# Optimization experiments

Measured on AMD Instinct MI355X. Metric: run time of the kernel, lower is better.

Reference implementation:

```python
import jax, jax.numpy as jnp
import numpy as np

B, T, C, H, HS = 128, 256, 384, 6, 64

def setup_inputs() -> dict:
    key = jax.random.key(0)
    k1, k2, k3, k4, k5 = jax.random.split(key, 5)
    s = 0.02
    return {
        "x": jax.random.normal(k1, (B, T, C), dtype=jnp.float32),
        "Wq": jax.random.normal(k2, (H, C, HS), dtype=jnp.float32) * s,
        "Wk": jax.random.normal(k3, (H, C, HS), dtype=jnp.float32) * s,
        "Wv": jax.random.normal(k4, (H, C, HS), dtype=jnp.float32) * s,
        "Wp": jax.random.normal(k5, (C, C), dtype=jnp.float32) * s,
        "bp": jnp.zeros((C,), dtype=jnp.float32),
    }

def reference(x, Wq, Wk, Wv, Wp, bp):
    # per-head projections: [B,H,T,HS]
    q = jnp.einsum('btc,hcd->bhtd', x, Wq)
    k = jnp.einsum('btc,hcd->bhtd', x, Wk)
    v = jnp.einsum('btc,hcd->bhtd', x, Wv)
    scale = 1.0 / jnp.sqrt(jnp.asarray(HS, dtype=x.dtype))
    # scores: [B,H,T,T], causal mask then stable softmax
    scores = jnp.einsum('bhtd,bhsd->bhts', q, k) * scale
    causal = jnp.tril(jnp.ones((T, T), dtype=bool))
    scores = jnp.where(causal, scores, -jnp.inf)
    wei = jax.nn.softmax(scores, axis=-1)
    # dropout is identity in eval mode
    out = jnp.einsum('bhts,bhsd->bhtd', wei, v)  # [B,H,T,HS]
    out = out.transpose(0, 2, 1, 3).reshape(B, T, H * HS)  # concat heads
    return out @ Wp.T + bp  # output projection
```

## Files before the change

kernel.cpp:

```cpp
#include <hip/hip_runtime.h>
#include <hip/hip_bf16.h>
#include <math.h>

#define B_   128
#define T_   256
#define C_   384
#define H_   6
#define HS_  64
#define NTOK (B_*T_)
#define NQKV (3*C_)

typedef unsigned short u16;
typedef __attribute__((ext_vector_type(8))) short bf16x8;
typedef __attribute__((ext_vector_type(4))) float f32x4;

__device__ __forceinline__ u16 f2b(float f) {
    unsigned int u = __builtin_bit_cast(unsigned int, f);
    unsigned int r = (u + 0x7FFFu + ((u >> 16) & 1u)) >> 16;
    return (u16)r;
}

__device__ __forceinline__ float fexp2(float x) {
#if __has_builtin(__builtin_amdgcn_exp2f)
    return __builtin_amdgcn_exp2f(x);
#else
    return exp2f(x);
#endif
}

__device__ __forceinline__ void gl2lds16(const u16* g, u16* l) {
    __builtin_amdgcn_global_load_lds(
        (const __attribute__((address_space(1))) unsigned int*)g,
        (__attribute__((address_space(3))) unsigned int*)l, 16, 0, 0);
}

#define QSCALE 0.180336880f

#define J0_ (NTOK*C_/8)
#define J2_ (C_*C_/8)
#define J1_ (NQKV*C_)

__global__ __launch_bounds__(256) void prep(
    const float* __restrict__ x,  const float* __restrict__ Wq,
    const float* __restrict__ Wk, const float* __restrict__ Wv,
    const float* __restrict__ Wp,
    u16* __restrict__ xb, u16* __restrict__ wct, u16* __restrict__ wpb)
{
    int i = blockIdx.x * 256 + threadIdx.x;
    if (i < J0_) {
        const float4* s = (const float4*)x + (size_t)i * 2;
        float4 a = s[0], b = s[1];
        ushort4 o1, o2;
        o1.x = f2b(a.x); o1.y = f2b(a.y); o1.z = f2b(a.z); o1.w = f2b(a.w);
        o2.x = f2b(b.x); o2.y = f2b(b.y); o2.z = f2b(b.z); o2.w = f2b(b.w);
        ((ushort4*)xb)[(size_t)i * 2]     = o1;
        ((ushort4*)xb)[(size_t)i * 2 + 1] = o2;
    } else if (i < J0_ + J2_) {
        int j = i - J0_;
        const float4* s = (const float4*)Wp + (size_t)j * 2;
        float4 a = s[0], b = s[1];
        ushort4 o1, o2;
        o1.x = f2b(a.x); o1.y = f2b(a.y); o1.z = f2b(a.z); o1.w = f2b(a.w);
        o2.x = f2b(b.x); o2.y = f2b(b.y); o2.z = f2b(b.z); o2.w = f2b(b.w);
        ((ushort4*)wpb)[(size_t)j * 2]     = o1;
        ((ushort4*)wpb)[(size_t)j * 2 + 1] = o2;
    } else {
        int j = i - J0_ - J2_;
        if (j < J1_) {
            int n = j / C_, c = j % C_;
            int p = n / C_, rem = n % C_;
            int h = rem >> 6, d = rem & 63;
            const float* W = (p == 0 ? Wq : (p == 1 ? Wk : Wv));
            wct[j] = f2b(W[(h * C_ + c) * HS_ + d]);
        }
    }
}

__global__ __launch_bounds__(512, 4) void gemm_qkv(
    const u16* __restrict__ xb, const u16* __restrict__ wct,
    u16* __restrict__ qo, u16* __restrict__ ko, u16* __restrict__ vt)
{
    __shared__ __align__(16) u16 As[256 * 64];
    __shared__ __align__(16) u16 Bs[128 * 64];

    const int gid  = blockIdx.x;
    const int xcd  = gid & 7;
    const int j_   = gid >> 3;
    const int colb = j_ % 9;
    const int rowb = (j_ / 9) * 8 + xcd;
    const int m0g  = rowb * 256;
    const int n0g  = colb * 128;

    const int tid = threadIdx.x;
    const int w = tid >> 6, lane = tid & 63;
    const int lm = lane & 15, qd = lane >> 4;
    const int wm = (w >> 1) * 64, wn = (w & 1) * 64;

    const int schunk = (lane & 7) ^ ((lane >> 3) & 7);
    const u16* gA = xb  + (size_t)(m0g + w * 32 + (lane >> 3)) * C_ + schunk * 8;
    const u16* gB = wct + (size_t)(n0g + w * 16 + (lane >> 3)) * C_ + schunk * 8;
    u16* lA = &As[(w * 32) * 64];
    u16* lB = &Bs[(w * 16) * 64];

    f32x4 acc[4][4];
    #pragma unroll
    for (int mi = 0; mi < 4; ++mi)
        #pragma unroll
        for (int ni = 0; ni < 4; ++ni)
            acc[mi][ni] = (f32x4){0.f, 0.f, 0.f, 0.f};

    for (int k0 = 0; k0 < C_; k0 += 64) {
        __syncthreads();
        #pragma unroll
        for (int j = 0; j < 4; ++j)
            gl2lds16(gA + j * 8 * C_, lA + j * 8 * 64);
        #pragma unroll
        for (int j = 0; j < 2; ++j)
            gl2lds16(gB + j * 8 * C_, lB + j * 8 * 64);
        gA += 64; gB += 64;
        __syncthreads();

        #pragma unroll
        for (int ks = 0; ks < 2; ++ks) {
            bf16x8 af[4], bfr[4];
            #pragma unroll
            for (int mi = 0; mi < 4; ++mi) {
                const int row = wm + mi * 16 + lm;
                const int sl = (ks * 4 + qd) ^ (lm & 7);
                af[mi] = *(const bf16x8*)&As[row * 64 + sl * 8];
            }
            #pragma unroll
            for (int ni = 0; ni < 4; ++ni) {
                const int row = wn + ni * 16 + lm;
                const int sl = (ks * 4 + qd) ^ (lm & 7);
                bfr[ni] = *(const bf16x8*)&Bs[row * 64 + sl * 8];
            }
            #pragma unroll
            for (int mi = 0; mi < 4; ++mi)
                #pragma unroll
                for (int ni = 0; ni < 4; ++ni)
                    acc[mi][ni] = __builtin_amdgcn_mfma_f32_16x16x32_bf16(
                        af[mi], bfr[ni], acc[mi][ni], 0, 0, 0);
        }
    }

    const int bI = m0g >> 8;

    if (colb < 6) {
        u16* dst = (colb < 3) ? qo : ko;
        const float scl = (colb < 3) ? QSCALE : 1.0f;
        const int hBase = (colb % 3) * 2;
        u16 (*tb)[136] = (u16(*)[136])As;
        const int rloc = tid >> 3;
        #pragma unroll
        for (int mi = 0; mi < 4; ++mi) {
            __syncthreads();
            #pragma unroll
            for (int ni = 0; ni < 4; ++ni)
                #pragma unroll
                for (int r = 0; r < 4; ++r)
                    tb[(w >> 1) * 16 + qd * 4 + r][wn + ni * 16 + lm]
                        = f2b(acc[mi][ni][r] * scl);
            __syncthreads();
            const int t = (rloc >> 4) * 64 + mi * 16 + (rloc & 15);
            #pragma unroll
            for (int jj = 0; jj < 2; ++jj) {
                const int cc = (tid & 7) * 8 + jj * 64;
                const int h = hBase + (cc >> 6);
                bf16x8 vv = *(const bf16x8*)&tb[rloc][cc];
                *(bf16x8*)(dst + ((size_t)(bI * H_ + h) * T_ + t) * HS_ + (cc & 63)) = vv;
            }
        }
    } else {
        #pragma unroll
        for (int mi = 0; mi < 4; ++mi) {
            #pragma unroll
            for (int ni = 0; ni < 4; ++ni) {
                const int nn = (colb - 6) * 128 + wn + ni * 16 + lm;
                const int h = nn >> 6, d = nn & 63;
                const int t0 = wm + mi * 16 + qd * 4;
                ushort4 sv;
                sv.x = f2b(acc[mi][ni][0]); sv.y = f2b(acc[mi][ni][1]);
                sv.z = f2b(acc[mi][ni][2]); sv.w = f2b(acc[mi][ni][3]);
                *(ushort4*)(vt + ((size_t)(bI * H_ + h) * HS_ + d) * T_ + t0) = sv;
            }
        }
    }
}

__global__ __launch_bounds__(256, 3) void attn_mfma(
    const u16* __restrict__ q, const u16* __restrict__ k,
    const u16* __restrict__ vt, u16* __restrict__ yb)
{
    __shared__ __align__(16) u16 SM[128 * 64 + 64 * 128 + 4 * 16 * 72];
    u16* Ks = SM;
    u16* Vs = SM + 8192;
    u16* Ps = SM + 16384;

    const int bh = blockIdx.x;
    const int qt = blockIdx.y;
    const int b = bh / H_, h = bh % H_;
    const int tid = threadIdx.x, w = tid >> 6, lane = tid & 63;
    const int lm = lane & 15, qd = lane >> 4;

    const u16* qb = q  + (size_t)bh * T_ * HS_;
    const u16* kb = k  + (size_t)bh * T_ * HS_;
    const u16* vb = vt + (size_t)bh * HS_ * T_;

    const int t0 = qt * 128 + w * 16;

    bf16x8 aq[2][2];
    #pragma unroll
    for (int rg = 0; rg < 2; ++rg) {
        const u16* qrow = qb + (size_t)(t0 + rg * 64 + lm) * HS_;
        aq[rg][0] = *(const bf16x8*)(qrow + qd * 8);
        aq[rg][1] = *(const bf16x8*)(qrow + 32 + qd * 8);
    }

    f32x4 acc[2][4];
    float ms[2][4], ls[2][4];
    #pragma unroll
    for (int rg = 0; rg < 2; ++rg) {
        #pragma unroll
        for (int ni = 0; ni < 4; ++ni) acc[rg][ni] = (f32x4){0.f, 0.f, 0.f, 0.f};
        #pragma unroll
        for (int r = 0; r < 4; ++r) { ms[rg][r] = -INFINITY; ls[rg][r] = 0.f; }
    }

    u16* Pw = &Ps[w * 16 * 72];
    const int nph = qt + 1;

    for (int p = 0; p < nph; ++p) {
        if (p) __syncthreads();
        #pragma unroll
        for (int j = 0; j < 4; ++j) {
            const int row = w * 32 + j * 8 + (lane >> 3);
            const int c = (lane & 7) ^ (row & 7);
            gl2lds16(kb + (size_t)(p * 128 + row) * HS_ + c * 8,
                     &Ks[(w * 32 + j * 8) * 64]);
        }
        #pragma unroll
        for (int j = 0; j < 4; ++j) {
            const int d = w * 16 + j * 4 + (lane >> 4);
            const int c = (lane & 15) ^ (d & 15);
            gl2lds16(vb + (size_t)d * T_ + p * 128 + c * 8,
                     &Vs[(w * 16 + j * 4) * 128]);
        }
        __syncthreads();

        for (int kt2 = 0; kt2 < 2; ++kt2) {
            const int j0 = p * 128 + kt2 * 64;
            #pragma unroll
            for (int rg = 0; rg < 2; ++rg) {
                const int trg = t0 + rg * 64;
                if (j0 > trg + 15) continue;
                const bool needmask = (j0 + 63 > trg);

                f32x4 st[4];
                #pragma unroll
                for (int ni = 0; ni < 4; ++ni) st[ni] = (f32x4){0.f, 0.f, 0.f, 0.f};
                #pragma unroll
                for (int ks = 0; ks < 2; ++ks) {
                    #pragma unroll
                    for (int ni = 0; ni < 4; ++ni) {
                        const int lrow = kt2 * 64 + ni * 16 + lm;
                        const int sl = (ks * 4 + qd) ^ (lm & 7);
                        bf16x8 bk = *(const bf16x8*)&Ks[lrow * 64 + sl * 8];
                        st[ni] = __builtin_amdgcn_mfma_f32_16x16x32_bf16(
                            aq[rg][ks], bk, st[ni], 0, 0, 0);
                    }
                }

                float vals[4][4], rowmax[4];
                #pragma unroll
                for (int r = 0; r < 4; ++r) rowmax[r] = -INFINITY;
                #pragma unroll
                for (int ni = 0; ni < 4; ++ni) {
                    const int s_g = j0 + ni * 16 + lm;
                    #pragma unroll
                    for (int r = 0; r < 4; ++r) {
                        float sc = st[ni][r];
                        if (needmask) {
                            const int t_g = trg + qd * 4 + r;
                            sc = (s_g > t_g) ? -1e30f : sc;
                        }
                        vals[ni][r] = sc;
                        rowmax[r] = fmaxf(rowmax[r], sc);
                    }
                }
                #pragma unroll
                for (int msk = 1; msk <= 8; msk <<= 1)
                    #pragma unroll
                    for (int r = 0; r < 4; ++r)
                        rowmax[r] = fmaxf(rowmax[r], __shfl_xor(rowmax[r], msk, 64));

                float corr[4], rowsum[4];
                #pragma unroll
                for (int r = 0; r < 4; ++r) {
                    const float mn = fmaxf(ms[rg][r], rowmax[r]);
                    corr[r] = fexp2(ms[rg][r] - mn);
                    ms[rg][r] = mn;
                    rowsum[r] = 0.f;
                }
                #pragma unroll
                for (int ni = 0; ni < 4; ++ni) {
                    #pragma unroll
                    for (int r = 0; r < 4; ++r) {
                        const float pv = fexp2(vals[ni][r] - ms[rg][r]);
                        rowsum[r] += pv;
                        Pw[(qd * 4 + r) * 72 + ni * 16 + lm] = f2b(pv);
                    }
                }
                #pragma unroll
                for (int msk = 1; msk <= 8; msk <<= 1)
                    #pragma unroll
                    for (int r = 0; r < 4; ++r)
                        rowsum[r] += __shfl_xor(rowsum[r], msk, 64);
                #pragma unroll
                for (int r = 0; r < 4; ++r) ls[rg][r] = ls[rg][r] * corr[r] + rowsum[r];
                #pragma unroll
                for (int ni = 0; ni < 4; ++ni)
                    #pragma unroll
                    for (int r = 0; r < 4; ++r)
                        acc[rg][ni][r] *= corr[r];

                #pragma unroll
                for (int ks = 0; ks < 2; ++ks) {
                    bf16x8 pa = *(const bf16x8*)&Pw[lm * 72 + ks * 32 + qd * 8];
                    #pragma unroll
                    for (int ni = 0; ni < 4; ++ni) {
                        const int d = ni * 16 + lm;
                        const int c = (kt2 * 8 + ks * 4 + qd) ^ lm;
                        bf16x8 bv = *(const bf16x8*)&Vs[d * 128 + c * 8];
                        acc[rg][ni] = __builtin_amdgcn_mfma_f32_16x16x32_bf16(
                            pa, bv, acc[rg][ni], 0, 0, 0);
                    }
                }
            }
        }
    }

    __syncthreads();
    u16 (*yt)[72] = (u16(*)[72])SM;
    #pragma unroll
    for (int rg = 0; rg < 2; ++rg)
        #pragma unroll
        for (int r = 0; r < 4; ++r) {
            const float inv = 1.f / ls[rg][r];
            #pragma unroll
            for (int ni = 0; ni < 4; ++ni)
                yt[w * 16 + rg * 64 + qd * 4 + r][ni * 16 + lm]
                    = f2b(acc[rg][ni][r] * inv);
        }
    __syncthreads();
    #pragma unroll
    for (int rr = 0; rr < 4; ++rr) {
        const int row = rr * 32 + (tid >> 3);
        const int col = (tid & 7) * 8;
        bf16x8 vv = *(const bf16x8*)&yt[row][col];
        const int t_g = qt * 128 + row;
        *(bf16x8*)(yb + ((size_t)(b * T_ + t_g)) * C_ + h * 64 + col) = vv;
    }
}

__global__ __launch_bounds__(512, 4) void gemm_proj(
    const u16* __restrict__ yb, const u16* __restrict__ wpb,
    const float* __restrict__ bp, float* __restrict__ out)
{
    __shared__ __align__(16) u16 SMEM[256 * 64 + 128 * 64];
    u16* As = SMEM;
    u16* Bs = SMEM + 256 * 64;

    const int gid  = blockIdx.x;
    const int xcd  = gid & 7;
    const int j_   = gid >> 3;
    const int colb = j_ % 3;
    const int rowb = (j_ / 3) * 8 + xcd;
    const int m0g  = rowb * 256;
    const int n0g  = colb * 128;

    const int tid = threadIdx.x;
    const int w = tid >> 6, lane = tid & 63;
    const int lm = lane & 15, qd = lane >> 4;
    const int wm = (w >> 1) * 64, wn = (w & 1) * 64;

    const int schunk = (lane & 7) ^ ((lane >> 3) & 7);
    const u16* gA = yb  + (size_t)(m0g + w * 32 + (lane >> 3)) * C_ + schunk * 8;
    const u16* gB = wpb + (size_t)(n0g + w * 16 + (lane >> 3)) * C_ + schunk * 8;
    u16* lA = &As[(w * 32) * 64];
    u16* lB = &Bs[(w * 16) * 64];

    f32x4 acc[4][4];
    #pragma unroll
    for (int mi = 0; mi < 4; ++mi)
        #pragma unroll
        for (int ni = 0; ni < 4; ++ni)
            acc[mi][ni] = (f32x4){0.f, 0.f, 0.f, 0.f};

    for (int k0 = 0; k0 < C_; k0 += 64) {
        __syncthreads();
        #pragma unroll
        for (int j = 0; j < 4; ++j)
            gl2lds16(gA + j * 8 * C_, lA + j * 8 * 64);
        #pragma unroll
        for (int j = 0; j < 2; ++j)
            gl2lds16(gB + j * 8 * C_, lB + j * 8 * 64);
        gA += 64; gB += 64;
        __syncthreads();

        #pragma unroll
        for (int ks = 0; ks < 2; ++ks) {
            bf16x8 af[4], bfr[4];
            #pragma unroll
            for (int mi = 0; mi < 4; ++mi) {
                const int row = wm + mi * 16 + lm;
                const int sl = (ks * 4 + qd) ^ (lm & 7);
                af[mi] = *(const bf16x8*)&As[row * 64 + sl * 8];
            }
            #pragma unroll
            for (int ni = 0; ni < 4; ++ni) {
                const int row = wn + ni * 16 + lm;
                const int sl = (ks * 4 + qd) ^ (lm & 7);
                bfr[ni] = *(const bf16x8*)&Bs[row * 64 + sl * 8];
            }
            #pragma unroll
            for (int mi = 0; mi < 4; ++mi)
                #pragma unroll
                for (int ni = 0; ni < 4; ++ni)
                    acc[mi][ni] = __builtin_amdgcn_mfma_f32_16x16x32_bf16(
                        af[mi], bfr[ni], acc[mi][ni], 0, 0, 0);
        }
    }

    float bpv[4];
    #pragma unroll
    for (int ni = 0; ni < 4; ++ni) bpv[ni] = bp[n0g + wn + ni * 16 + lm];

    float (*tb)[132] = (float(*)[132])SMEM;
    const int rloc = tid >> 3;
    #pragma unroll
    for (int mi = 0; mi < 4; ++mi) {
        __syncthreads();
        #pragma unroll
        for (int ni = 0; ni < 4; ++ni)
            #pragma unroll
            for (int r = 0; r < 4; ++r)
                tb[(w >> 1) * 16 + qd * 4 + r][wn + ni * 16 + lm]
                    = acc[mi][ni][r] + bpv[ni];
        __syncthreads();
        const int m = m0g + (rloc >> 4) * 64 + mi * 16 + (rloc & 15);
        #pragma unroll
        for (int jj = 0; jj < 4; ++jj) {
            const int cc = (tid & 7) * 4 + jj * 32;
            float4 vv = *(const float4*)&tb[rloc][cc];
            *(float4*)(out + (size_t)m * C_ + n0g + cc) = vv;
        }
    }
}

extern "C" void kernel_launch(void* const* d_in, const int* in_sizes, int n_in,
                              void* d_out, int out_size, void* d_ws, size_t ws_size,
                              hipStream_t stream)
{
    const float* x  = (const float*)d_in[0];
    const float* Wq = (const float*)d_in[1];
    const float* Wk = (const float*)d_in[2];
    const float* Wv = (const float*)d_in[3];
    const float* Wp = (const float*)d_in[4];
    const float* bp = (const float*)d_in[5];
    float* out = (float*)d_out;

    u16* xb  = (u16*)d_ws;
    u16* wct = xb  + (size_t)NTOK * C_;
    u16* wpb = wct + (size_t)NQKV * C_;
    u16* qo  = wpb + (size_t)C_ * C_;
    u16* ko  = qo  + (size_t)B_ * H_ * T_ * HS_;
    u16* vt  = ko  + (size_t)B_ * H_ * T_ * HS_;
    u16* yb  = vt  + (size_t)B_ * H_ * T_ * HS_;

    const int prep_blocks = (J0_ + J2_ + J1_ + 255) / 256;
    hipLaunchKernelGGL(prep, dim3(prep_blocks), dim3(256), 0, stream,
                       x, Wq, Wk, Wv, Wp, xb, wct, wpb);

    hipLaunchKernelGGL(gemm_qkv, dim3((NTOK / 256) * (NQKV / 128)), dim3(512), 0, stream,
                       xb, wct, qo, ko, vt);

    hipLaunchKernelGGL(attn_mfma, dim3(B_ * H_, T_ / 128), dim3(256), 0, stream,
                       qo, ko, vt, yb);

    hipLaunchKernelGGL(gemm_proj, dim3((NTOK / 256) * (C_ / 128)), dim3(512), 0, stream,
                       yb, wpb, bp, out);
}
```

Measured before the change: 197.5 us.

## Fuse QKV projection and causal attention into one per-(batch,head) kernel

Merges the QKV GEMM and the attention kernel so each block computes Q, K and V for one (batch, head) over all 256 tokens. The results stay in shared memory with swizzled layouts instead of round-tripping through global memory. The weight layout is reordered per head (q,k,v contiguous per head) so one block's B tile covers 192 columns. This removes the intermediate Q/K/V global writes and reads and one launch, but uses 96KB of LDS, fewer blocks (768), lower occupancy, and causal imbalance between warps.

```diff
diff --git a/kernel.cpp b/kernel.cpp
--- a/kernel.cpp
+++ b/kernel.cpp
@@ -68,45 +68,43 @@
         int j = i - J0_ - J2_;
         if (j < J1_) {
             int n = j / C_, c = j % C_;
-            int p = n / C_, rem = n % C_;
-            int h = rem >> 6, d = rem & 63;
+            int h = n / 192, rem = n % 192;
+            int p = rem >> 6, d = rem & 63;
             const float* W = (p == 0 ? Wq : (p == 1 ? Wk : Wv));
             wct[j] = f2b(W[(h * C_ + c) * HS_ + d]);
         }
     }
 }
 
-__global__ __launch_bounds__(512, 4) void gemm_qkv(
+__global__ __launch_bounds__(512, 2) void qkv_attn(
     const u16* __restrict__ xb, const u16* __restrict__ wct,
-    u16* __restrict__ qo, u16* __restrict__ ko, u16* __restrict__ vt)
+    u16* __restrict__ yb)
 {
-    __shared__ __align__(16) u16 As[256 * 64];
-    __shared__ __align__(16) u16 Bs[128 * 64];
-
-    const int gid  = blockIdx.x;
-    const int xcd  = gid & 7;
-    const int j_   = gid >> 3;
-    const int colb = j_ % 9;
-    const int rowb = (j_ / 9) * 8 + xcd;
-    const int m0g  = rowb * 256;
-    const int n0g  = colb * 128;
+    __shared__ __align__(16) u16 SM[49152];
+    u16* Qs = SM;
+    u16* Ks = SM + 16384;
+    u16* Vs = SM + 32768;
+
+    const int gid = blockIdx.x;
+    const int lin = (gid & 7) * 96 + (gid >> 3);
+    const int b = lin / 6, h = lin % 6;
 
     const int tid = threadIdx.x;
     const int w = tid >> 6, lane = tid & 63;
     const int lm = lane & 15, qd = lane >> 4;
-    const int wm = (w >> 1) * 64, wn = (w & 1) * 64;
+    const int wm = (w >> 1) * 64, wn = (w & 1) * 96;
 
     const int schunk = (lane & 7) ^ ((lane >> 3) & 7);
-    const u16* gA = xb  + (size_t)(m0g + w * 32 + (lane >> 3)) * C_ + schunk * 8;
-    const u16* gB = wct + (size_t)(n0g + w * 16 + (lane >> 3)) * C_ + schunk * 8;
-    u16* lA = &As[(w * 32) * 64];
-    u16* lB = &Bs[(w * 16) * 64];
-
-    f32x4 acc[4][4];
+    const u16* gA = xb  + (size_t)(b * T_ + w * 32 + (lane >> 3)) * C_ + schunk * 8;
+    const u16* gB = wct + (size_t)(h * 192 + w * 24 + (lane >> 3)) * C_ + schunk * 8;
+    u16* lA = &Qs[(w * 32) * 64];
+    u16* lB = &Ks[(w * 24) * 64];
+
+    f32x4 acc[4][6];
     #pragma unroll
     for (int mi = 0; mi < 4; ++mi)
         #pragma unroll
-        for (int ni = 0; ni < 4; ++ni)
+        for (int ni = 0; ni < 6; ++ni)
             acc[mi][ni] = (f32x4){0.f, 0.f, 0.f, 0.f};
 
     for (int k0 = 0; k0 < C_; k0 += 64) {
@@ -115,226 +113,180 @@
         for (int j = 0; j < 4; ++j)
             gl2lds16(gA + j * 8 * C_, lA + j * 8 * 64);
         #pragma unroll
-        for (int j = 0; j < 2; ++j)
+        for (int j = 0; j < 3; ++j)
             gl2lds16(gB + j * 8 * C_, lB + j * 8 * 64);
         gA += 64; gB += 64;
         __syncthreads();
 
         #pragma unroll
         for (int ks = 0; ks < 2; ++ks) {
-            bf16x8 af[4], bfr[4];
+            bf16x8 af[4], bfr[6];
             #pragma unroll
             for (int mi = 0; mi < 4; ++mi) {
                 const int row = wm + mi * 16 + lm;
                 const int sl = (ks * 4 + qd) ^ (lm & 7);
-                af[mi] = *(const bf16x8*)&As[row * 64 + sl * 8];
-            }
-            #pragma unroll
-            for (int ni = 0; ni < 4; ++ni) {
+                af[mi] = *(const bf16x8*)&Qs[row * 64 + sl * 8];
+            }
+            #pragma unroll
+            for (int ni = 0; ni < 6; ++ni) {
                 const int row = wn + ni * 16 + lm;
                 const int sl = (ks * 4 + qd) ^ (lm & 7);
-                bfr[ni] = *(const bf16x8*)&Bs[row * 64 + sl * 8];
+                bfr[ni] = *(const bf16x8*)&Ks[row * 64 + sl * 8];
             }
             #pragma unroll
             for (int mi = 0; mi < 4; ++mi)
                 #pragma unroll
-                for (int ni = 0; ni < 4; ++ni)
+                for (int ni = 0; ni < 6; ++ni)
                     acc[mi][ni] = __builtin_amdgcn_mfma_f32_16x16x32_bf16(
                         af[mi], bfr[ni], acc[mi][ni], 0, 0, 0);
         }
     }
 
-    const int bI = m0g >> 8;
-
-    if (colb < 6) {
-        u16* dst = (colb < 3) ? qo : ko;
-        const float scl = (colb < 3) ? QSCALE : 1.0f;
-        const int hBase = (colb % 3) * 2;
-        u16 (*tb)[136] = (u16(*)[136])As;
-        const int rloc = tid >> 3;
-        #pragma unroll
-        for (int mi = 0; mi < 4; ++mi) {
-            __syncthreads();
-            #pragma unroll
-            for (int ni = 0; ni < 4; ++ni)
-                #pragma unroll
-                for (int r = 0; r < 4; ++r)
-                    tb[(w >> 1) * 16 + qd * 4 + r][wn + ni * 16 + lm]
-                        = f2b(acc[mi][ni][r] * scl);
-            __syncthreads();
-            const int t = (rloc >> 4) * 64 + mi * 16 + (rloc & 15);
-            #pragma unroll
-            for (int jj = 0; jj < 2; ++jj) {
-                const int cc = (tid & 7) * 8 + jj * 64;
-                const int h = hBase + (cc >> 6);
-                bf16x8 vv = *(const bf16x8*)&tb[rloc][cc];
-                *(bf16x8*)(dst + ((size_t)(bI * H_ + h) * T_ + t) * HS_ + (cc & 63)) = vv;
-            }
-        }
-    } else {
-        #pragma unroll
-        for (int mi = 0; mi < 4; ++mi) {
-            #pragma unroll
-            for (int ni = 0; ni < 4; ++ni) {
-                const int nn = (colb - 6) * 128 + wn + ni * 16 + lm;
-                const int h = nn >> 6, d = nn & 63;
-                const int t0 = wm + mi * 16 + qd * 4;
+    __syncthreads();
+    #pragma unroll
+    for (int mi = 0; mi < 4; ++mi) {
+        const int t0 = wm + mi * 16 + qd * 4;
+        #pragma unroll
+        for (int ni = 0; ni < 6; ++ni) {
+            const int n = wn + ni * 16 + lm;
+            if (n < 64) {
+                #pragma unroll
+                for (int r = 0; r < 4; ++r) {
+                    const int t = t0 + r;
+                    Qs[t * 64 + (((n >> 3) ^ (t & 7)) << 3) + (n & 7)]
+                        = f2b(acc[mi][ni][r] * QSCALE);
+                }
+            } else if (n < 128) {
+                const int d = n - 64;
+                #pragma unroll
+                for (int r = 0; r < 4; ++r) {
+                    const int t = t0 + r;
+                    Ks[t * 64 + (((d >> 3) ^ (t & 7)) << 3) + (d & 7)]
+                        = f2b(acc[mi][ni][r]);
+                }
+            } else {
+                const int d = n - 128;
+                const int ch = t0 >> 3;
+                const int pos = (ch & 16) | ((ch ^ (d & 15)) & 15);
                 ushort4 sv;
                 sv.x = f2b(acc[mi][ni][0]); sv.y = f2b(acc[mi][ni][1]);
                 sv.z = f2b(acc[mi][ni][2]); sv.w = f2b(acc[mi][ni][3]);
-                *(ushort4*)(vt + ((size_t)(bI * H_ + h) * HS_ + d) * T_ + t0) = sv;
-            }
-        }
-    }
-}
-
-__global__ __launch_bounds__(256, 3) void attn_mfma(
-    const u16* __restrict__ q, const u16* __restrict__ k,
-    const u16* __restrict__ vt, u16* __restrict__ yb)
-{
-    __shared__ __align__(16) u16 SM[128 * 64 + 64 * 128 + 4 * 16 * 72];
-    u16* Ks = SM;
-    u16* Vs = SM + 8192;
-    u16* Ps = SM + 16384;
-
-    const int bh = blockIdx.x;
-    const int qt = blockIdx.y;
-    const int b = bh / H_, h = bh % H_;
-    const int tid = threadIdx.x, w = tid >> 6, lane = tid & 63;
-    const int lm = lane & 15, qd = lane >> 4;
-
-    const u16* qb = q  + (size_t)bh * T_ * HS_;
-    const u16* kb = k  + (size_t)bh * T_ * HS_;
-    const u16* vb = vt + (size_t)bh * HS_ * T_;
-
-    const int t0 = qt * 128 + w * 16;
+                *(ushort4*)&Vs[d * 256 + pos * 8 + (t0 & 7)] = sv;
+            }
+        }
+    }
+    __syncthreads();
 
     bf16x8 aq[2][2];
     #pragma unroll
     for (int rg = 0; rg < 2; ++rg) {
-        const u16* qrow = qb + (size_t)(t0 + rg * 64 + lm) * HS_;
-        aq[rg][0] = *(const bf16x8*)(qrow + qd * 8);
-        aq[rg][1] = *(const bf16x8*)(qrow + 32 + qd * 8);
-    }
-
-    f32x4 acc[2][4];
+        const int t = rg * 128 + w * 16 + lm;
+        #pragma unroll
+        for (int ks = 0; ks < 2; ++ks)
+            aq[rg][ks] = *(const bf16x8*)
+                &Qs[t * 64 + (((ks * 4 + qd) ^ (t & 7)) << 3)];
+    }
+    __syncthreads();
+
+    f32x4 oacc[2][4];
     float ms[2][4], ls[2][4];
     #pragma unroll
     for (int rg = 0; rg < 2; ++rg) {
         #pragma unroll
-        for (int ni = 0; ni < 4; ++ni) acc[rg][ni] = (f32x4){0.f, 0.f, 0.f, 0.f};
+        for (int ni = 0; ni < 4; ++ni) oacc[rg][ni] = (f32x4){0.f, 0.f, 0.f, 0.f};
         #pragma unroll
         for (int r = 0; r < 4; ++r) { ms[rg][r] = -INFINITY; ls[rg][r] = 0.f; }
     }
 
-    u16* Pw = &Ps[w * 16 * 72];
-    const int nph = qt + 1;
-
-    for (int p = 0; p < nph; ++p) {
-        if (p) __syncthreads();
-        #pragma unroll
-        for (int j = 0; j < 4; ++j) {
-            const int row = w * 32 + j * 8 + (lane >> 3);
-            const int c = (lane & 7) ^ (row & 7);
-            gl2lds16(kb + (size_t)(p * 128 + row) * HS_ + c * 8,
-                     &Ks[(w * 32 + j * 8) * 64]);
-        }
-        #pragma unroll
-        for (int j = 0; j < 4; ++j) {
-            const int d = w * 16 + j * 4 + (lane >> 4);
-            const int c = (lane & 15) ^ (d & 15);
-            gl2lds16(vb + (size_t)d * T_ + p * 128 + c * 8,
-                     &Vs[(w * 16 + j * 4) * 128]);
-        }
-        __syncthreads();
-
-        for (int kt2 = 0; kt2 < 2; ++kt2) {
-            const int j0 = p * 128 + kt2 * 64;
-            #pragma unroll
-            for (int rg = 0; rg < 2; ++rg) {
-                const int trg = t0 + rg * 64;
-                if (j0 > trg + 15) continue;
-                const bool needmask = (j0 + 63 > trg);
-
-                f32x4 st[4];
-                #pragma unroll
-                for (int ni = 0; ni < 4; ++ni) st[ni] = (f32x4){0.f, 0.f, 0.f, 0.f};
-                #pragma unroll
-                for (int ks = 0; ks < 2; ++ks) {
-                    #pragma unroll
-                    for (int ni = 0; ni < 4; ++ni) {
-                        const int lrow = kt2 * 64 + ni * 16 + lm;
-                        const int sl = (ks * 4 + qd) ^ (lm & 7);
-                        bf16x8 bk = *(const bf16x8*)&Ks[lrow * 64 + sl * 8];
-                        st[ni] = __builtin_amdgcn_mfma_f32_16x16x32_bf16(
-                            aq[rg][ks], bk, st[ni], 0, 0, 0);
+    u16* Pw = SM + w * (16 * 72);
+
+    #pragma unroll
+    for (int rg = 0; rg < 2; ++rg) {
+        const int trg = rg * 128 + w * 16;
+        const int kmax = (trg + 15) >> 6;
+        for (int kt = 0; kt <= kmax; ++kt) {
+            const int j0 = kt * 64;
+            const bool needmask = (j0 + 63 > trg);
+
+            f32x4 st[4];
+            #pragma unroll
+            for (int ni = 0; ni < 4; ++ni) st[ni] = (f32x4){0.f, 0.f, 0.f, 0.f};
+            #pragma unroll
+            for (int ks = 0; ks < 2; ++ks) {
+                #pragma unroll
+                for (int ni = 0; ni < 4; ++ni) {
+                    const int krow = j0 + ni * 16 + lm;
+                    const int sl = (ks * 4 + qd) ^ (lm & 7);
+                    bf16x8 bk = *(const bf16x8*)&Ks[krow * 64 + sl * 8];
+                    st[ni] = __builtin_amdgcn_mfma_f32_16x16x32_bf16(
+                        aq[rg][ks], bk, st[ni], 0, 0, 0);
+                }
+            }
+
+            float vals[4][4], rowmax[4];
+            #pragma unroll
+            for (int r = 0; r < 4; ++r) rowmax[r] = -INFINITY;
+            #pragma unroll
+            for (int ni = 0; ni < 4; ++ni) {
+                const int s_g = j0 + ni * 16 + lm;
+                #pragma unroll
+                for (int r = 0; r < 4; ++r) {
+                    float sc = st[ni][r];
+                    if (needmask) {
+                        const int t_g = trg + qd * 4 + r;
+                        sc = (s_g > t_g) ? -1e30f : sc;
                     }
-                }
-
-                float vals[4][4], rowmax[4];
-                #pragma unroll
-                for (int r = 0; r < 4; ++r) rowmax[r] = -INFINITY;
+                    vals[ni][r] = sc;
+                    rowmax[r] = fmaxf(rowmax[r], sc);
+                }
+            }
+            #pragma unroll
+            for (int msk = 1; msk <= 8; msk <<= 1)
+                #pragma unroll
+                for (int r = 0; r < 4; ++r)
+                    rowmax[r] = fmaxf(rowmax[r], __shfl_xor(rowmax[r], msk, 64));
+
+            float corr[4], rowsum[4];
+            #pragma unroll
+            for (int r = 0; r < 4; ++r) {
+                const float mn = fmaxf(ms[rg][r], rowmax[r]);
+                corr[r] = fexp2(ms[rg][r] - mn);
+                ms[rg][r] = mn;
+                rowsum[r] = 0.f;
+            }
+            #pragma unroll
+            for (int ni = 0; ni < 4; ++ni) {
+                #pragma unroll
+                for (int r = 0; r < 4; ++r) {
+                    const float pv = fexp2(vals[ni][r] - ms[rg][r]);
+                    rowsum[r] += pv;
+                    Pw[(qd * 4 + r) * 72 + ni * 16 + lm] = f2b(pv);
+                }
+            }
+            #pragma unroll
+            for (int msk = 1; msk <= 8; msk <<= 1)
+                #pragma unroll
+                for (int r = 0; r < 4; ++r)
+                    rowsum[r] += __shfl_xor(rowsum[r], msk, 64);
+            #pragma unroll
+            for (int r = 0; r < 4; ++r) ls[rg][r] = ls[rg][r] * corr[r] + rowsum[r];
+            #pragma unroll
+            for (int ni = 0; ni < 4; ++ni)
+                #pragma unroll
+                for (int r = 0; r < 4; ++r)
+                    oacc[rg][ni][r] *= corr[r];
+
+            #pragma unroll
+            for (int ks = 0; ks < 2; ++ks) {
+                bf16x8 pa = *(const bf16x8*)&Pw[lm * 72 + ks * 32 + qd * 8];
                 #pragma unroll
                 for (int ni = 0; ni < 4; ++ni) {
-                    const int s_g = j0 + ni * 16 + lm;
-                    #pragma unroll
-                    for (int r = 0; r < 4; ++r) {
-                        float sc = st[ni][r];
-                        if (needmask) {
-                            const int t_g = trg + qd * 4 + r;
-                            sc = (s_g > t_g) ? -1e30f : sc;
-                        }
-                        vals[ni][r] = sc;
-                        rowmax[r] = fmaxf(rowmax[r], sc);
-                    }
-                }
-                #pragma unroll
-                for (int msk = 1; msk <= 8; msk <<= 1)
-                    #pragma unroll
-                    for (int r = 0; r < 4; ++r)
-                        rowmax[r] = fmaxf(rowmax[r], __shfl_xor(rowmax[r], msk, 64));
-
-                float corr[4], rowsum[4];
-                #pragma unroll
-                for (int r = 0; r < 4; ++r) {
-                    const float mn = fmaxf(ms[rg][r], rowmax[r]);
-                    corr[r] = fexp2(ms[rg][r] - mn);
-                    ms[rg][r] = mn;
-                    rowsum[r] = 0.f;
-                }
-                #pragma unroll
-                for (int ni = 0; ni < 4; ++ni) {
-                    #pragma unroll
-                    for (int r = 0; r < 4; ++r) {
-                        const float pv = fexp2(vals[ni][r] - ms[rg][r]);
-                        rowsum[r] += pv;
-                        Pw[(qd * 4 + r) * 72 + ni * 16 + lm] = f2b(pv);
-                    }
-                }
-                #pragma unroll
-                for (int msk = 1; msk <= 8; msk <<= 1)
-                    #pragma unroll
-                    for (int r = 0; r < 4; ++r)
-                        rowsum[r] += __shfl_xor(rowsum[r], msk, 64);
-                #pragma unroll
-                for (int r = 0; r < 4; ++r) ls[rg][r] = ls[rg][r] * corr[r] + rowsum[r];
-                #pragma unroll
-                for (int ni = 0; ni < 4; ++ni)
-                    #pragma unroll
-                    for (int r = 0; r < 4; ++r)
-                        acc[rg][ni][r] *= corr[r];
-
-                #pragma unroll
-                for (int ks = 0; ks < 2; ++ks) {
-                    bf16x8 pa = *(const bf16x8*)&Pw[lm * 72 + ks * 32 + qd * 8];
-                    #pragma unroll
-                    for (int ni = 0; ni < 4; ++ni) {
-                        const int d = ni * 16 + lm;
-                        const int c = (kt2 * 8 + ks * 4 + qd) ^ lm;
-                        bf16x8 bv = *(const bf16x8*)&Vs[d * 128 + c * 8];
-                        acc[rg][ni] = __builtin_amdgcn_mfma_f32_16x16x32_bf16(
-                            pa, bv, acc[rg][ni], 0, 0, 0);
-                    }
+                    const int d = ni * 16 + lm;
+                    const int cj = kt * 8 + ks * 4 + qd;
+                    const int pos = (cj & 16) | ((cj ^ (d & 15)) & 15);
+                    bf16x8 bv = *(const bf16x8*)&Vs[d * 256 + pos * 8];
+                    oacc[rg][ni] = __builtin_amdgcn_mfma_f32_16x16x32_bf16(
+                        pa, bv, oacc[rg][ni], 0, 0, 0);
                 }
             }
         }
@@ -343,23 +295,23 @@
     __syncthreads();
     u16 (*yt)[72] = (u16(*)[72])SM;
     #pragma unroll
-    for (int rg = 0; rg < 2; ++rg)
+    for (int rg = 0; rg < 2; ++rg) {
+        const int trow = rg * 128 + w * 16 + qd * 4;
         #pragma unroll
         for (int r = 0; r < 4; ++r) {
             const float inv = 1.f / ls[rg][r];
             #pragma unroll
             for (int ni = 0; ni < 4; ++ni)
-                yt[w * 16 + rg * 64 + qd * 4 + r][ni * 16 + lm]
-                    = f2b(acc[rg][ni][r] * inv);
-        }
+                yt[trow + r][ni * 16 + lm] = f2b(oacc[rg][ni][r] * inv);
+        }
+    }
     __syncthreads();
     #pragma unroll
     for (int rr = 0; rr < 4; ++rr) {
-        const int row = rr * 32 + (tid >> 3);
+        const int row = rr * 64 + (tid >> 3);
         const int col = (tid & 7) * 8;
         bf16x8 vv = *(const bf16x8*)&yt[row][col];
-        const int t_g = qt * 128 + row;
-        *(bf16x8*)(yb + ((size_t)(b * T_ + t_g)) * C_ + h * 64 + col) = vv;
+        *(bf16x8*)(yb + ((size_t)(b * T_ + row)) * C_ + h * 64 + col) = vv;
     }
 }
 
@@ -473,20 +425,14 @@
     u16* xb  = (u16*)d_ws;
     u16* wct = xb  + (size_t)NTOK * C_;
     u16* wpb = wct + (size_t)NQKV * C_;
-    u16* qo  = wpb + (size_t)C_ * C_;
-    u16* ko  = qo  + (size_t)B_ * H_ * T_ * HS_;
-    u16* vt  = ko  + (size_t)B_ * H_ * T_ * HS_;
-    u16* yb  = vt  + (size_t)B_ * H_ * T_ * HS_;
+    u16* yb  = wpb + (size_t)C_ * C_;
 
     const int prep_blocks = (J0_ + J2_ + J1_ + 255) / 256;
     hipLaunchKernelGGL(prep, dim3(prep_blocks), dim3(256), 0, stream,
                        x, Wq, Wk, Wv, Wp, xb, wct, wpb);
 
-    hipLaunchKernelGGL(gemm_qkv, dim3((NTOK / 256) * (NQKV / 128)), dim3(512), 0, stream,
-                       xb, wct, qo, ko, vt);
-
-    hipLaunchKernelGGL(attn_mfma, dim3(B_ * H_, T_ / 128), dim3(256), 0, stream,
-                       qo, ko, vt, yb);
+    hipLaunchKernelGGL(qkv_attn, dim3(B_ * H_), dim3(512), 0, stream,
+                       xb, wct, yb);
 
     hipLaunchKernelGGL(gemm_proj, dim3((NTOK / 256) * (C_ / 128)), dim3(512), 0, stream,
                        yb, wpb, bp, out);
```

Result: faster. 187.9 us (-4.9%).
